# Kernel tuning notes

Hardware: AMD Instinct MI355X
Metric: run time of the kernel (lower is better)

## Reference

```python
import jax, jax.numpy as jnp
import numpy as np

N_NODES = 100000
N_EDGES = 1000000
DIMS = [64, 64, 64, 64]  # neurons_per_layer -> 3 ConvLayers


def _glorot(key, shape):
    fan_in, fan_out = shape[1], shape[0]
    limit = float(np.sqrt(6.0 / (fan_in + fan_out)))
    return jax.random.uniform(key, shape, jnp.float32, -limit, limit)


def setup_inputs() -> dict:
    key = jax.random.key(0)
    ks = jax.random.split(key, 3 + 3 * len(DIMS))
    inp = {
        "x": jax.random.normal(ks[0], (N_NODES, DIMS[0]), jnp.float32),
        "edge_index": jax.random.randint(ks[1], (2, N_EDGES), 0, N_NODES, jnp.int64),
        "edge_weight": jax.random.uniform(ks[2], (N_EDGES,), jnp.float32),
    }
    for i in range(len(DIMS) - 1):
        din, dout = DIMS[i], DIMS[i + 1]
        inp[f"Wl{i}"] = _glorot(ks[3 + 3 * i], (dout, din))
        inp[f"bl{i}"] = jnp.zeros((dout,), jnp.float32)
        inp[f"Wr{i}"] = _glorot(ks[4 + 3 * i], (dout, din))
    return inp


def conv_layer(x, row, col, edge_weight, Wl, bl, Wr):
    n = x.shape[0]
    # symmetric degree normalization of edge weights
    deg = jax.ops.segment_sum(edge_weight, col, num_segments=n)
    dis = jnp.where(deg > 0, jax.lax.rsqrt(jnp.where(deg > 0, deg, 1.0)), 0.0)
    w = dis[row] * edge_weight * dis[col]
    # weighted messages, mean aggregation at target nodes
    msg = w[:, None] * x[row]                                    # [E, d]
    agg = jax.ops.segment_sum(msg, col, num_segments=n)          # [N, d]
    cnt = jax.ops.segment_sum(jnp.ones_like(edge_weight), col, num_segments=n)
    agg = agg / jnp.maximum(cnt, 1.0)[:, None]
    # lin_l(agg) + lin_r(x)
    return agg @ Wl.T + bl + x @ Wr.T


def reference(x, edge_index, edge_weight, Wl0, bl0, Wr0, Wl1, bl1, Wr1, Wl2, bl2, Wr2):
    row, col = edge_index[0], edge_index[1]
    params = [(Wl0, bl0, Wr0), (Wl1, bl1, Wr1), (Wl2, bl2, Wr2)]
    h = x
    for i, (Wl, bl, Wr) in enumerate(params):
        h = conv_layer(h, row, col, edge_weight, Wl, bl, Wr)
        if i != len(params) - 1:
            h = jax.nn.relu(h)
    return h
```

## Files before the change

### kernel.cpp

```cpp
#include <hip/hip_runtime.h>


static constexpr int kD = 64;
static constexpr int WPAD = 68;
typedef unsigned int uint_t;
typedef unsigned short ushort_t;

__device__ __forceinline__ float bf2f(ushort_t u) {
  return __uint_as_float(((uint_t)u) << 16);
}
__device__ __forceinline__ ushort_t f2bf(float f) {
  uint_t u = __float_as_uint(f);
  u += 0x7fffu + ((u >> 16) & 1u);
  return (ushort_t)(u >> 16);
}

__global__ __launch_bounds__(256) void k_edge_deg(
    const int* __restrict__ col, const float* __restrict__ ew,
    float* __restrict__ deg, uint_t* __restrict__ cnt, int E) {
  int e = blockIdx.x * 256 + threadIdx.x;
  if (e >= E) return;
  int c = col[e];
  unsafeAtomicAdd(&deg[c], ew[e]);
  atomicAdd(&cnt[c], 1u);
}

__global__ __launch_bounds__(256) void k_node_pre(float* __restrict__ deg, int N) {
  int n = blockIdx.x * 256 + threadIdx.x;
  if (n >= N) return;
  float d = deg[n];
  deg[n] = (d > 0.0f) ? rsqrtf(d) : 0.0f;
}

__global__ __launch_bounds__(256) void k_scanA(
    const uint_t* __restrict__ cnt, uint_t* __restrict__ incl,
    uint_t* __restrict__ bsum, int N) {
  __shared__ uint_t s[256];
  int t = threadIdx.x;
  int i = blockIdx.x * 256 + t;
  uint_t v = (i < N) ? cnt[i] : 0u;
  s[t] = v;
  __syncthreads();
  for (int off = 1; off < 256; off <<= 1) {
    uint_t tv = (t >= off) ? s[t - off] : 0u;
    __syncthreads();
    s[t] += tv;
    __syncthreads();
  }
  if (i < N) incl[i] = s[t];
  if (t == 255) bsum[blockIdx.x] = s[255];
}

__global__ __launch_bounds__(512) void k_scanB(
    const uint_t* __restrict__ bsum, uint_t* __restrict__ boff, int nb) {
  __shared__ uint_t s[512];
  int t = threadIdx.x;
  uint_t v = (t < nb) ? bsum[t] : 0u;
  s[t] = v;
  __syncthreads();
  for (int off = 1; off < 512; off <<= 1) {
    uint_t tv = (t >= off) ? s[t - off] : 0u;
    __syncthreads();
    s[t] += tv;
    __syncthreads();
  }
  if (t < nb) boff[t] = s[t] - v;
}

__global__ __launch_bounds__(256) void k_scanC(
    const uint_t* __restrict__ incl, const uint_t* __restrict__ cnt,
    const uint_t* __restrict__ boff, uint_t* __restrict__ rowptr, int N) {
  int i = blockIdx.x * 256 + threadIdx.x;
  if (i >= N) return;
  uint_t inc = incl[i] + boff[i >> 8];
  rowptr[i] = inc - cnt[i];
  if (i == N - 1) rowptr[N] = inc;
}

__global__ __launch_bounds__(256) void k_fill(
    const int* __restrict__ row, const int* __restrict__ col,
    const float* __restrict__ ew, const float* __restrict__ dis,
    const uint_t* __restrict__ rowptr, uint_t* __restrict__ fillcnt,
    int2* __restrict__ csr, int E) {
  int e = blockIdx.x * 256 + threadIdx.x;
  if (e >= E) return;
  int c = col[e];
  int r = row[e];
  float w = dis[r] * ew[e] * dis[c];
  uint_t pos = atomicAdd(&fillcnt[c], 1u);
  csr[rowptr[c] + pos] = make_int2(r, __float_as_int(w));
}

__global__ __launch_bounds__(256) void k_cvt(
    const float* __restrict__ x, ushort_t* __restrict__ xb, int total) {
  int i = blockIdx.x * 256 + threadIdx.x;
  if (i >= total) return;
  xb[i] = f2bf(x[i]);
}

__global__ __launch_bounds__(512) void k_layer(
    const ushort_t* __restrict__ A, ushort_t* __restrict__ B16,
    float* __restrict__ Bf,
    const int2* __restrict__ csr, const uint_t* __restrict__ rowptr,
    const float* __restrict__ Wl, const float* __restrict__ bl,
    const float* __restrict__ Wr, int N, int relu, int nwaves) {
  __shared__ float sW[2 * kD * WPAD];
  __shared__ float sAgg[8][kD];
  __shared__ float sX[8][kD];
  int tid = threadIdx.x;
  int wave = tid >> 6, lane = tid & 63;
  int g = lane >> 4;
  int l16 = lane & 15;

  for (int i = tid; i < kD * 16; i += 512) {
    int r = i >> 4, c4 = i & 15;
    float4 v = reinterpret_cast<const float4*>(Wl)[i];
    float4 u = reinterpret_cast<const float4*>(Wr)[i];
    *reinterpret_cast<float4*>(&sW[r * WPAD + c4 * 4]) = v;
    *reinterpret_cast<float4*>(&sW[kD * WPAD + r * WPAD + c4 * 4]) = u;
  }
  float bias = bl[lane];
  __syncthreads();

  const float* sWl = sW + (size_t)lane * WPAD;
  const float* sWr = sW + kD * WPAD + (size_t)lane * WPAD;

  int gw = blockIdx.x * 8 + wave;
  for (int n = gw; n < N; n += nwaves) {
    uint_t rb = rowptr[n];
    uint_t re = rowptr[n + 1];
    int degc = (int)(re - rb);
    float4 acc = make_float4(0.f, 0.f, 0.f, 0.f);
    for (uint_t base = rb; base < re; base += 64) {
      int m = (int)min(64u, re - base);
      int2 erw = (lane < m) ? csr[base + lane] : make_int2(0, 0);
      int steps = (m + 3) >> 2;
      int i = 0;
#define GATHER_ONE(S, ACC)                                                     \
      {                                                                        \
        int rr = __shfl(erw.x, (S));                                           \
        float ww = __int_as_float(__shfl(erw.y, (S)));                         \
        uint2 q = *reinterpret_cast<const uint2*>(A + (size_t)rr * kD + l16 * 4); \
        float f0 = __uint_as_float(q.x << 16);                                 \
        float f1 = __uint_as_float(q.x & 0xffff0000u);                         \
        float f2 = __uint_as_float(q.y << 16);                                 \
        float f3 = __uint_as_float(q.y & 0xffff0000u);                         \
        ACC.x += ww * f0; ACC.y += ww * f1; ACC.z += ww * f2; ACC.w += ww * f3; \
      }
      for (; i + 4 <= steps; i += 4) {
        GATHER_ONE(i * 4 + g, acc)
        GATHER_ONE(i * 4 + 4 + g, acc)
        GATHER_ONE(i * 4 + 8 + g, acc)
        GATHER_ONE(i * 4 + 12 + g, acc)
      }
      for (; i < steps; ++i) {
        GATHER_ONE(i * 4 + g, acc)
      }
#undef GATHER_ONE
    }
    acc.x += __shfl_xor(acc.x, 16); acc.y += __shfl_xor(acc.y, 16);
    acc.z += __shfl_xor(acc.z, 16); acc.w += __shfl_xor(acc.w, 16);
    acc.x += __shfl_xor(acc.x, 32); acc.y += __shfl_xor(acc.y, 32);
    acc.z += __shfl_xor(acc.z, 32); acc.w += __shfl_xor(acc.w, 32);
    float ci = (degc > 0) ? (1.0f / (float)degc) : 1.0f;
    if (g == 0) {
      *reinterpret_cast<float4*>(&sAgg[wave][l16 * 4]) =
          make_float4(acc.x * ci, acc.y * ci, acc.z * ci, acc.w * ci);
    }
    sX[wave][lane] = bf2f(A[(size_t)n * kD + lane]);
    float o = bias;
#pragma unroll
    for (int k4 = 0; k4 < 16; ++k4) {
      float4 ag = *reinterpret_cast<const float4*>(&sAgg[wave][k4 * 4]);
      float4 xv = *reinterpret_cast<const float4*>(&sX[wave][k4 * 4]);
      float4 wl = *reinterpret_cast<const float4*>(&sWl[k4 * 4]);
      float4 wr = *reinterpret_cast<const float4*>(&sWr[k4 * 4]);
      o += ag.x * wl.x + ag.y * wl.y + ag.z * wl.z + ag.w * wl.w;
      o += xv.x * wr.x + xv.y * wr.y + xv.z * wr.z + xv.w * wr.w;
    }
    if (relu) o = fmaxf(o, 0.0f);
    if (B16) B16[(size_t)n * kD + lane] = f2bf(o);
    else     Bf[(size_t)n * kD + lane] = o;
  }
}

extern "C" void kernel_launch(void* const* d_in, const int* in_sizes, int n_in,
                              void* d_out, int out_size, void* d_ws, size_t ws_size,
                              hipStream_t stream) {
  const float* x   = (const float*)d_in[0];
  const int*   ei  = (const int*)d_in[1];
  const float* ew  = (const float*)d_in[2];
  const float* Wl0 = (const float*)d_in[3];
  const float* bl0 = (const float*)d_in[4];
  const float* Wr0 = (const float*)d_in[5];
  const float* Wl1 = (const float*)d_in[6];
  const float* bl1 = (const float*)d_in[7];
  const float* Wr1 = (const float*)d_in[8];
  const float* Wl2 = (const float*)d_in[9];
  const float* bl2 = (const float*)d_in[10];
  const float* Wr2 = (const float*)d_in[11];
  float* out = (float*)d_out;

  const int N = in_sizes[0] / kD;
  const int E = in_sizes[2];
  const int* row = ei;
  const int* col = ei + E;

  const int nb256 = (N + 255) / 256;

  char* p = (char*)d_ws;
  int2*     csr     = (int2*)p;     p += (size_t)E * sizeof(int2);
  ushort_t* xb      = (ushort_t*)p; p += (size_t)N * kD * sizeof(ushort_t);
  ushort_t* h1      = (ushort_t*)p; p += (size_t)N * kD * sizeof(ushort_t);
  ushort_t* h2      = (ushort_t*)p; p += (size_t)N * kD * sizeof(ushort_t);
  float*    deg     = (float*)p;    p += (size_t)N * sizeof(float);
  uint_t*   cnt     = (uint_t*)p;   p += (size_t)N * sizeof(uint_t);
  uint_t*   fillcnt = (uint_t*)p;   p += (size_t)N * sizeof(uint_t);
  uint_t*   rowptr  = (uint_t*)p;   p += (size_t)(N + 1) * sizeof(uint_t);
  uint_t*   incl    = (uint_t*)p;   p += (size_t)N * sizeof(uint_t);
  uint_t*   bsum    = (uint_t*)p;   p += (size_t)nb256 * sizeof(uint_t);
  uint_t*   boff    = (uint_t*)p;

  const int eb = (E + 255) / 256;

  hipMemsetAsync(deg, 0, 3 * (size_t)N * sizeof(float), stream);
  k_edge_deg<<<eb, 256, 0, stream>>>(col, ew, deg, cnt, E);
  k_node_pre<<<nb256, 256, 0, stream>>>(deg, N);
  k_scanA<<<nb256, 256, 0, stream>>>(cnt, incl, bsum, N);
  k_scanB<<<1, 512, 0, stream>>>(bsum, boff, nb256);
  k_scanC<<<nb256, 256, 0, stream>>>(incl, cnt, boff, rowptr, N);
  k_fill<<<eb, 256, 0, stream>>>(row, col, ew, deg, rowptr, fillcnt, csr, E);
  k_cvt<<<(N * kD + 255) / 256, 256, 0, stream>>>(x, xb, N * kD);

  const int blocks = 1024;
  const int nwaves = blocks * 8;
  k_layer<<<blocks, 512, 0, stream>>>(xb, h1, nullptr, csr, rowptr, Wl0, bl0, Wr0, N, 1, nwaves);
  k_layer<<<blocks, 512, 0, stream>>>(h1, h2, nullptr, csr, rowptr, Wl1, bl1, Wr1, N, 1, nwaves);
  k_layer<<<blocks, 512, 0, stream>>>(h2, nullptr, out, csr, rowptr, Wl2, bl2, Wr2, N, 0, nwaves);
}
```

Before: 666.8 us.

## Hold layer weights in registers and gather edges directly per lane group

Each lane now keeps its row of Wl and Wr in 128 registers instead of reading them from padded shared memory. The per-wave staging of aggregated and self features in LDS switches to bf16 to cut shared traffic. The edge loop now loads CSR entries directly per lane-group with predication, replacing the coalesced load plus shuffle broadcast, and blocks shrink to 256 threads. The register-resident weights raise VGPR pressure and may reduce occupancy or spill. Rounding the aggregate to bf16 also adds precision loss.

```diff
diff --git a/kernel.cpp b/kernel.cpp
--- a/kernel.cpp
+++ b/kernel.cpp
@@ -2,13 +2,9 @@
 
 
 static constexpr int kD = 64;
-static constexpr int WPAD = 68;
 typedef unsigned int uint_t;
 typedef unsigned short ushort_t;
 
-__device__ __forceinline__ float bf2f(ushort_t u) {
-  return __uint_as_float(((uint_t)u) << 16);
-}
 __device__ __forceinline__ ushort_t f2bf(float f) {
   uint_t u = __float_as_uint(f);
   u += 0x7fffu + ((u >> 16) & 1u);
@@ -98,85 +94,82 @@
   xb[i] = f2bf(x[i]);
 }
 
-__global__ __launch_bounds__(512) void k_layer(
+__global__ __launch_bounds__(256) void k_layer(
     const ushort_t* __restrict__ A, ushort_t* __restrict__ B16,
     float* __restrict__ Bf,
     const int2* __restrict__ csr, const uint_t* __restrict__ rowptr,
     const float* __restrict__ Wl, const float* __restrict__ bl,
     const float* __restrict__ Wr, int N, int relu, int nwaves) {
-  __shared__ float sW[2 * kD * WPAD];
-  __shared__ float sAgg[8][kD];
-  __shared__ float sX[8][kD];
+  __shared__ ushort_t sAggB[4][kD];
+  __shared__ ushort_t sXb[4][kD];
   int tid = threadIdx.x;
   int wave = tid >> 6, lane = tid & 63;
   int g = lane >> 4;
   int l16 = lane & 15;
 
-  for (int i = tid; i < kD * 16; i += 512) {
-    int r = i >> 4, c4 = i & 15;
-    float4 v = reinterpret_cast<const float4*>(Wl)[i];
-    float4 u = reinterpret_cast<const float4*>(Wr)[i];
-    *reinterpret_cast<float4*>(&sW[r * WPAD + c4 * 4]) = v;
-    *reinterpret_cast<float4*>(&sW[kD * WPAD + r * WPAD + c4 * 4]) = u;
+  float4 wl4[16], wr4[16];
+#pragma unroll
+  for (int k = 0; k < 16; ++k) {
+    wl4[k] = *reinterpret_cast<const float4*>(Wl + (size_t)lane * kD + k * 4);
+    wr4[k] = *reinterpret_cast<const float4*>(Wr + (size_t)lane * kD + k * 4);
   }
   float bias = bl[lane];
-  __syncthreads();
-
-  const float* sWl = sW + (size_t)lane * WPAD;
-  const float* sWr = sW + kD * WPAD + (size_t)lane * WPAD;
-
-  int gw = blockIdx.x * 8 + wave;
+
+  int gw = blockIdx.x * 4 + wave;
   for (int n = gw; n < N; n += nwaves) {
     uint_t rb = rowptr[n];
     uint_t re = rowptr[n + 1];
     int degc = (int)(re - rb);
     float4 acc = make_float4(0.f, 0.f, 0.f, 0.f);
-    for (uint_t base = rb; base < re; base += 64) {
-      int m = (int)min(64u, re - base);
-      int2 erw = (lane < m) ? csr[base + lane] : make_int2(0, 0);
-      int steps = (m + 3) >> 2;
-      int i = 0;
-#define GATHER_ONE(S, ACC)                                                     \
-      {                                                                        \
-        int rr = __shfl(erw.x, (S));                                           \
-        float ww = __int_as_float(__shfl(erw.y, (S)));                         \
-        uint2 q = *reinterpret_cast<const uint2*>(A + (size_t)rr * kD + l16 * 4); \
-        float f0 = __uint_as_float(q.x << 16);                                 \
-        float f1 = __uint_as_float(q.x & 0xffff0000u);                         \
-        float f2 = __uint_as_float(q.y << 16);                                 \
-        float f3 = __uint_as_float(q.y & 0xffff0000u);                         \
-        ACC.x += ww * f0; ACC.y += ww * f1; ACC.z += ww * f2; ACC.w += ww * f3; \
-      }
-      for (; i + 4 <= steps; i += 4) {
-        GATHER_ONE(i * 4 + g, acc)
-        GATHER_ONE(i * 4 + 4 + g, acc)
-        GATHER_ONE(i * 4 + 8 + g, acc)
-        GATHER_ONE(i * 4 + 12 + g, acc)
-      }
-      for (; i < steps; ++i) {
-        GATHER_ONE(i * 4 + g, acc)
-      }
-#undef GATHER_ONE
+#define GATHER_STEP(IDX)                                                   \
+    { uint_t ix = (IDX);                                                   \
+      bool val = ix < re;                                                  \
+      int2 er = csr[val ? ix : rb];                                        \
+      float ww = val ? __int_as_float(er.y) : 0.0f;                        \
+      uint2 q = *reinterpret_cast<const uint2*>(A + (size_t)er.x * kD + l16 * 4); \
+      acc.x += ww * __uint_as_float(q.x << 16);                            \
+      acc.y += ww * __uint_as_float(q.x & 0xffff0000u);                    \
+      acc.z += ww * __uint_as_float(q.y << 16);                            \
+      acc.w += ww * __uint_as_float(q.y & 0xffff0000u); }
+    for (uint_t s4 = rb + g; s4 < re; s4 += 8) {
+      GATHER_STEP(s4)
+      GATHER_STEP(s4 + 4)
     }
+#undef GATHER_STEP
     acc.x += __shfl_xor(acc.x, 16); acc.y += __shfl_xor(acc.y, 16);
     acc.z += __shfl_xor(acc.z, 16); acc.w += __shfl_xor(acc.w, 16);
     acc.x += __shfl_xor(acc.x, 32); acc.y += __shfl_xor(acc.y, 32);
     acc.z += __shfl_xor(acc.z, 32); acc.w += __shfl_xor(acc.w, 32);
     float ci = (degc > 0) ? (1.0f / (float)degc) : 1.0f;
     if (g == 0) {
-      *reinterpret_cast<float4*>(&sAgg[wave][l16 * 4]) =
-          make_float4(acc.x * ci, acc.y * ci, acc.z * ci, acc.w * ci);
+      uint_t p0 = (uint_t)f2bf(acc.x * ci) | ((uint_t)f2bf(acc.y * ci) << 16);
+      uint_t p1 = (uint_t)f2bf(acc.z * ci) | ((uint_t)f2bf(acc.w * ci) << 16);
+      *reinterpret_cast<uint2*>(&sAggB[wave][l16 * 4]) = make_uint2(p0, p1);
     }
-    sX[wave][lane] = bf2f(A[(size_t)n * kD + lane]);
+    sXb[wave][lane] = A[(size_t)n * kD + lane];
     float o = bias;
 #pragma unroll
-    for (int k4 = 0; k4 < 16; ++k4) {
-      float4 ag = *reinterpret_cast<const float4*>(&sAgg[wave][k4 * 4]);
-      float4 xv = *reinterpret_cast<const float4*>(&sX[wave][k4 * 4]);
-      float4 wl = *reinterpret_cast<const float4*>(&sWl[k4 * 4]);
-      float4 wr = *reinterpret_cast<const float4*>(&sWr[k4 * 4]);
-      o += ag.x * wl.x + ag.y * wl.y + ag.z * wl.z + ag.w * wl.w;
-      o += xv.x * wr.x + xv.y * wr.y + xv.z * wr.z + xv.w * wr.w;
+    for (int k8 = 0; k8 < 8; ++k8) {
+      uint4 qa = *reinterpret_cast<const uint4*>(&sAggB[wave][k8 * 8]);
+      uint4 qx = *reinterpret_cast<const uint4*>(&sXb[wave][k8 * 8]);
+      float4 wla = wl4[k8 * 2], wlb = wl4[k8 * 2 + 1];
+      float4 wra = wr4[k8 * 2], wrb = wr4[k8 * 2 + 1];
+      o += __uint_as_float(qa.x << 16)         * wla.x;
+      o += __uint_as_float(qa.x & 0xffff0000u) * wla.y;
+      o += __uint_as_float(qa.y << 16)         * wla.z;
+      o += __uint_as_float(qa.y & 0xffff0000u) * wla.w;
+      o += __uint_as_float(qa.z << 16)         * wlb.x;
+      o += __uint_as_float(qa.z & 0xffff0000u) * wlb.y;
+      o += __uint_as_float(qa.w << 16)         * wlb.z;
+      o += __uint_as_float(qa.w & 0xffff0000u) * wlb.w;
+      o += __uint_as_float(qx.x << 16)         * wra.x;
+      o += __uint_as_float(qx.x & 0xffff0000u) * wra.y;
+      o += __uint_as_float(qx.y << 16)         * wra.z;
+      o += __uint_as_float(qx.y & 0xffff0000u) * wra.w;
+      o += __uint_as_float(qx.z << 16)         * wrb.x;
+      o += __uint_as_float(qx.z & 0xffff0000u) * wrb.y;
+      o += __uint_as_float(qx.w << 16)         * wrb.z;
+      o += __uint_as_float(qx.w & 0xffff0000u) * wrb.w;
     }
     if (relu) o = fmaxf(o, 0.0f);
     if (B16) B16[(size_t)n * kD + lane] = f2bf(o);
@@ -232,9 +225,9 @@
   k_fill<<<eb, 256, 0, stream>>>(row, col, ew, deg, rowptr, fillcnt, csr, E);
   k_cvt<<<(N * kD + 255) / 256, 256, 0, stream>>>(x, xb, N * kD);
 
-  const int blocks = 1024;
-  const int nwaves = blocks * 8;
-  k_layer<<<blocks, 512, 0, stream>>>(xb, h1, nullptr, csr, rowptr, Wl0, bl0, Wr0, N, 1, nwaves);
-  k_layer<<<blocks, 512, 0, stream>>>(h1, h2, nullptr, csr, rowptr, Wl1, bl1, Wr1, N, 1, nwaves);
-  k_layer<<<blocks, 512, 0, stream>>>(h2, nullptr, out, csr, rowptr, Wl2, bl2, Wr2, N, 0, nwaves);
-}
+  const int blocks = 2048;
+  const int nwaves = blocks * 4;
+  k_layer<<<blocks, 256, 0, stream>>>(xb, h1, nullptr, csr, rowptr, Wl0, bl0, Wr0, N, 1, nwaves);
+  k_layer<<<blocks, 256, 0, stream>>>(h1, h2, nullptr, csr, rowptr, Wl1, bl1, Wr1, N, 1, nwaves);
+  k_layer<<<blocks, 256, 0, stream>>>(h2, nullptr, out, csr, rowptr, Wl2, bl2, Wr2, N, 0, nwaves);
+}
```

Measured after the change: 721.2 us. 8.2% more time.

## Process two nodes per wave with interleaved edge gathers

Applied to the files above, without the earlier changes.

Each wave now handles a pair of destination nodes, interleaving their neighbor gathers so more independent memory loads are in flight. Edge entries are loaded directly per lane group instead of being loaded once per 64-edge chunk and broadcast with shuffles. The aim is to hide gather latency for low-degree nodes, where the average degree is about ten. In exchange, lanes waste loads on padded steps when the two degrees differ, and each lane re-reads CSR entries, raising per-lane load count.

```diff
diff --git a/kernel.cpp b/kernel.cpp
--- a/kernel.cpp
+++ b/kernel.cpp
@@ -125,63 +125,67 @@
   const float* sWl = sW + (size_t)lane * WPAD;
   const float* sWr = sW + kD * WPAD + (size_t)lane * WPAD;
 
+  int npairs = (N + 1) >> 1;
   int gw = blockIdx.x * 8 + wave;
-  for (int n = gw; n < N; n += nwaves) {
-    uint_t rb = rowptr[n];
-    uint_t re = rowptr[n + 1];
-    int degc = (int)(re - rb);
-    float4 acc = make_float4(0.f, 0.f, 0.f, 0.f);
-    for (uint_t base = rb; base < re; base += 64) {
-      int m = (int)min(64u, re - base);
-      int2 erw = (lane < m) ? csr[base + lane] : make_int2(0, 0);
-      int steps = (m + 3) >> 2;
-      int i = 0;
-#define GATHER_ONE(S, ACC)                                                     \
-      {                                                                        \
-        int rr = __shfl(erw.x, (S));                                           \
-        float ww = __int_as_float(__shfl(erw.y, (S)));                         \
-        uint2 q = *reinterpret_cast<const uint2*>(A + (size_t)rr * kD + l16 * 4); \
-        float f0 = __uint_as_float(q.x << 16);                                 \
-        float f1 = __uint_as_float(q.x & 0xffff0000u);                         \
-        float f2 = __uint_as_float(q.y << 16);                                 \
-        float f3 = __uint_as_float(q.y & 0xffff0000u);                         \
-        ACC.x += ww * f0; ACC.y += ww * f1; ACC.z += ww * f2; ACC.w += ww * f3; \
-      }
-      for (; i + 4 <= steps; i += 4) {
-        GATHER_ONE(i * 4 + g, acc)
-        GATHER_ONE(i * 4 + 4 + g, acc)
-        GATHER_ONE(i * 4 + 8 + g, acc)
-        GATHER_ONE(i * 4 + 12 + g, acc)
-      }
-      for (; i < steps; ++i) {
-        GATHER_ONE(i * 4 + g, acc)
-      }
-#undef GATHER_ONE
+
+#define GATHER_STEP(IX, RE, RB, ACC)                                           \
+    { uint_t ix = (IX);                                                        \
+      bool val = ix < (RE);                                                    \
+      int2 er = csr[val ? ix : (RB)];                                          \
+      float ww = val ? __int_as_float(er.y) : 0.0f;                            \
+      uint2 q = *reinterpret_cast<const uint2*>(A + (size_t)er.x * kD + l16 * 4); \
+      ACC.x += ww * __uint_as_float(q.x << 16);                                \
+      ACC.y += ww * __uint_as_float(q.x & 0xffff0000u);                        \
+      ACC.z += ww * __uint_as_float(q.y << 16);                                \
+      ACC.w += ww * __uint_as_float(q.y & 0xffff0000u); }
+
+#define REDUCE_TRANSFORM(ACC, NN, DEGC)                                        \
+    { ACC.x += __shfl_xor(ACC.x, 16); ACC.y += __shfl_xor(ACC.y, 16);          \
+      ACC.z += __shfl_xor(ACC.z, 16); ACC.w += __shfl_xor(ACC.w, 16);          \
+      ACC.x += __shfl_xor(ACC.x, 32); ACC.y += __shfl_xor(ACC.y, 32);          \
+      ACC.z += __shfl_xor(ACC.z, 32); ACC.w += __shfl_xor(ACC.w, 32);          \
+      float ci = ((DEGC) > 0) ? (1.0f / (float)(DEGC)) : 1.0f;                 \
+      if (g == 0) {                                                            \
+        *reinterpret_cast<float4*>(&sAgg[wave][l16 * 4]) =                     \
+            make_float4(ACC.x * ci, ACC.y * ci, ACC.z * ci, ACC.w * ci);       \
+      }                                                                        \
+      sX[wave][lane] = bf2f(A[(size_t)(NN) * kD + lane]);                      \
+      float o = bias;                                                          \
+      _Pragma("unroll")                                                        \
+      for (int k4 = 0; k4 < 16; ++k4) {                                        \
+        float4 ag = *reinterpret_cast<const float4*>(&sAgg[wave][k4 * 4]);     \
+        float4 xv = *reinterpret_cast<const float4*>(&sX[wave][k4 * 4]);       \
+        float4 wl = *reinterpret_cast<const float4*>(&sWl[k4 * 4]);            \
+        float4 wr = *reinterpret_cast<const float4*>(&sWr[k4 * 4]);            \
+        o += ag.x * wl.x + ag.y * wl.y + ag.z * wl.z + ag.w * wl.w;            \
+        o += xv.x * wr.x + xv.y * wr.y + xv.z * wr.z + xv.w * wr.w;            \
+      }                                                                        \
+      if (relu) o = fmaxf(o, 0.0f);                                            \
+      if (B16) B16[(size_t)(NN) * kD + lane] = f2bf(o);                        \
+      else     Bf[(size_t)(NN) * kD + lane] = o; }
+
+  for (int pp = gw; pp < npairs; pp += nwaves) {
+    int n0 = pp * 2;
+    int n1 = n0 + 1;
+    bool has1 = n1 < N;
+    uint_t rb0 = rowptr[n0], re0 = rowptr[n0 + 1];
+    uint_t rb1 = has1 ? rowptr[n1] : 0u;
+    uint_t re1 = has1 ? rowptr[n1 + 1] : 0u;
+    int deg0 = (int)(re0 - rb0);
+    int deg1 = (int)(re1 - rb1);
+    float4 acc0 = make_float4(0.f, 0.f, 0.f, 0.f);
+    float4 acc1 = make_float4(0.f, 0.f, 0.f, 0.f);
+    for (uint_t i0 = rb0 + g, i1 = rb1 + g; i0 < re0 || i1 < re1; i0 += 8, i1 += 8) {
+      GATHER_STEP(i0,     re0, rb0, acc0)
+      GATHER_STEP(i1,     re1, rb1, acc1)
+      GATHER_STEP(i0 + 4, re0, rb0, acc0)
+      GATHER_STEP(i1 + 4, re1, rb1, acc1)
     }
-    acc.x += __shfl_xor(acc.x, 16); acc.y += __shfl_xor(acc.y, 16);
-    acc.z += __shfl_xor(acc.z, 16); acc.w += __shfl_xor(acc.w, 16);
-    acc.x += __shfl_xor(acc.x, 32); acc.y += __shfl_xor(acc.y, 32);
-    acc.z += __shfl_xor(acc.z, 32); acc.w += __shfl_xor(acc.w, 32);
-    float ci = (degc > 0) ? (1.0f / (float)degc) : 1.0f;
-    if (g == 0) {
-      *reinterpret_cast<float4*>(&sAgg[wave][l16 * 4]) =
-          make_float4(acc.x * ci, acc.y * ci, acc.z * ci, acc.w * ci);
-    }
-    sX[wave][lane] = bf2f(A[(size_t)n * kD + lane]);
-    float o = bias;
-#pragma unroll
-    for (int k4 = 0; k4 < 16; ++k4) {
-      float4 ag = *reinterpret_cast<const float4*>(&sAgg[wave][k4 * 4]);
-      float4 xv = *reinterpret_cast<const float4*>(&sX[wave][k4 * 4]);
-      float4 wl = *reinterpret_cast<const float4*>(&sWl[k4 * 4]);
-      float4 wr = *reinterpret_cast<const float4*>(&sWr[k4 * 4]);
-      o += ag.x * wl.x + ag.y * wl.y + ag.z * wl.z + ag.w * wl.w;
-      o += xv.x * wr.x + xv.y * wr.y + xv.z * wr.z + xv.w * wr.w;
-    }
-    if (relu) o = fmaxf(o, 0.0f);
-    if (B16) B16[(size_t)n * kD + lane] = f2bf(o);
-    else     Bf[(size_t)n * kD + lane] = o;
-  }
+    REDUCE_TRANSFORM(acc0, n0, deg0)
+    if (has1) REDUCE_TRANSFORM(acc1, n1, deg1)
+  }
+#undef GATHER_STEP
+#undef REDUCE_TRANSFORM
 }
 
 extern "C" void kernel_launch(void* const* d_in, const int* in_sizes, int n_in,
```

Result: no change. 678.2 us (+1.7%).
